# Kernel tuning notes

Hardware: AMD Instinct MI355X
Metric: run time of the kernel (lower is better)

The kernel has to match this reference:

```python
import jax, jax.numpy as jnp
import numpy as np

N = 20000      # nodes
E = 320000     # edges
GD = 256       # g_dim
H = 8          # head_n
D = 32         # head_d
XD = 256       # x_dim
PS = 4         # x_ps
HID = 512      # FF hidden (hardcoded in module)
EPS = 1e-5
SCALE = GD ** -0.5  # note: module scales by g_dim**-0.5, not head_d**-0.5


def layernorm(x, w, b):
    mu = jnp.mean(x, axis=-1, keepdims=True)
    var = jnp.var(x, axis=-1, keepdims=True)
    return (x - mu) * jax.lax.rsqrt(var + EPS) * w + b


def setup_inputs() -> dict:
    key = jax.random.key(0)
    ks = jax.random.split(key, 16)
    inp = {
        "x": jax.random.normal(ks[0], (N, XD, PS, PS), jnp.float32),
        "h": jax.random.normal(ks[1], (N, GD), jnp.float32),
        "src": jax.random.randint(ks[2], (E,), 0, N, jnp.int32),
        "dst": jax.random.randint(ks[3], (E,), 0, N, jnp.int32),
        # xproj conv (kernel covers full patch -> equivalent to a linear)
        "conv_w": jax.random.normal(ks[4], (GD, XD, PS, PS), jnp.float32) * 0.02,
        "conv_b": jnp.zeros((GD,), jnp.float32),
        # GraphT outer LayerNorm
        "norm_w": jnp.ones((GD,), jnp.float32),
        "norm_b": jnp.zeros((GD,), jnp.float32),
        # attention norm_in + projections
        "nin_w": jnp.ones((GD,), jnp.float32),
        "nin_b": jnp.zeros((GD,), jnp.float32),
        "w_qkv": jax.random.normal(ks[5], (3 * H * D, GD), jnp.float32) * 0.02,
        "w_out": jax.random.normal(ks[6], (GD, H * D), jnp.float32) * 0.02,
        "b_out": jnp.zeros((GD,), jnp.float32),
        # FeedForward: LayerNorm + Linear(GD,HID) + GELU + Linear(HID,GD)
        "ffn_w": jnp.ones((GD,), jnp.float32),
        "ffn_b": jnp.zeros((GD,), jnp.float32),
        "w1": jax.random.normal(ks[7], (HID, GD), jnp.float32) * 0.02,
        "b1": jnp.zeros((HID,), jnp.float32),
        "w2": jax.random.normal(ks[8], (GD, HID), jnp.float32) * 0.02,
        "b2": jnp.zeros((GD,), jnp.float32),
    }
    return inp


def reference(x, h, src, dst, conv_w, conv_b, norm_w, norm_b, nin_w, nin_b,
              w_qkv, w_out, b_out, ffn_w, ffn_b, w1, b1, w2, b2):
    # xproj: Conv2d with kernel == full spatial extent -> linear over flattened patch
    xp = x.reshape(N, XD * PS * PS) @ conv_w.reshape(GD, XD * PS * PS).T + conv_b  # [N, GD]

    hn = layernorm(h, norm_w, norm_b)  # GraphT.norm

    # --- GraphAttention ---
    s = layernorm(hn, nin_w, nin_b)                    # norm_in
    qkv = s @ w_qkv.T                                  # [N, 3*H*D]
    q, k, v = jnp.split(qkv, 3, axis=-1)
    q = q.reshape(N, H, D)
    k = k.reshape(N, H, D)
    v = v.reshape(N, H, D)

    # per-edge elementwise attention (DGL u_mul_v), scaled
    att = q[src] * k[dst] * SCALE                      # [E, H, D]
    # edge softmax over incoming edges of each destination, per (h, d) slot
    amax = jax.ops.segment_max(att, dst, num_segments=N)   # [N, H, D]
    e = jnp.exp(att - amax[dst])
    z = jax.ops.segment_sum(e, dst, num_segments=N)
    a = e / z[dst]                                     # [E, H, D]
    # weighted aggregation: sum over edges of v_src * att
    rst = jax.ops.segment_sum(v[src] * a, dst, num_segments=N)  # [N, H, D]

    attn_out = rst.reshape(N, H * D) @ w_out.T + b_out  # to_out (dropout=eval noop)

    # --- FeedForward (norm -> linear -> gelu -> linear) ---
    f = layernorm(attn_out, ffn_w, ffn_b)
    f = jax.nn.gelu(f @ w1.T + b1, approximate=False)
    f = f @ w2.T + b2

    out = f + hn + xp
    return out
```

## Files before the change

### kernel.cpp

```cpp
#include <hip/hip_runtime.h>
#include <hip/hip_bf16.h>
#include <math.h>

typedef __hip_bfloat16 bf16;
typedef __attribute__((ext_vector_type(8))) short bf16x8;
typedef __attribute__((ext_vector_type(4))) float f32x4;

#define N_NODES 20000
#define N_EDGES 320000
#define GD 256
#define HID 512
#define QKV3 768
#define XK 4096
#define SCALE 0.0625f
#define EPS 1e-5f

__device__ __forceinline__ float b2f(bf16 x) { return __bfloat162float(x); }
__device__ __forceinline__ bf16 f2b(float x) { return __float2bfloat16(x); }
__device__ __forceinline__ short f2bs(float x) {
    bf16 b = __float2bfloat16(x);
    union { bf16 b; short s; } u; u.b = b; return u.s;
}
__device__ __forceinline__ float ldf(const void* p, size_t i, int isbf) {
    return isbf ? __bfloat162float(((const bf16*)p)[i]) : ((const float*)p)[i];
}

typedef __attribute__((address_space(3))) void lds_void;
typedef __attribute__((address_space(1))) void glb_void;
__device__ __forceinline__ void gload_lds16(const void* g, void* l) {
    __builtin_amdgcn_global_load_lds((const glb_void*)g, (lds_void*)l, 16, 0, 0);
}

__global__ void detect_kernel(const void* __restrict__ normw, int* __restrict__ flag) {
    if (threadIdx.x == 0) {
        unsigned short u = ((const unsigned short*)normw)[0];
        *flag = (u == 0x3F80) ? 1 : 0;
    }
}

struct ConvArgs {
    const void* src[5];
    bf16* dst[5];
    int n[5];
};
__global__ void conv_bf16_all(ConvArgs a, const int* __restrict__ flag, bf16* __restrict__ cwt) {
    int i = blockIdx.x * 256 + threadIdx.x;
    int fl = *flag;
    #pragma unroll
    for (int s = 0; s < 5; ++s) {
        if (i < a.n[s]) {
            float v = ldf(a.src[s], i, fl);
            a.dst[s][i] = f2b(v);
            if (s == 0) {
                int r = i >> 12;
                int k = i & 4095;
                int T = k >> 5, slot = (k >> 3) & 3, e = k & 7;
                cwt[((size_t)T << 13) + (slot << 11) + (r << 3) + e] = f2b(v);
            }
            return;
        }
        i -= a.n[s];
    }
}

__global__ void count_kernel(const int* __restrict__ dst, int* __restrict__ deg) {
    int e = blockIdx.x * 256 + threadIdx.x;
    if (e < N_EDGES) atomicAdd(&deg[dst[e]], 1);
}

__global__ void scan_kernel(const int* __restrict__ deg, int* __restrict__ offsets,
                            int* __restrict__ cursor) {
    const int T = 1024;
    int t = threadIdx.x;
    int chunk = (N_NODES + T - 1) / T;
    int beg = t * chunk;
    int end = beg + chunk; if (end > N_NODES) end = N_NODES;
    int s = 0;
    for (int i = beg; i < end; ++i) s += deg[i];
    __shared__ int ls[T];
    ls[t] = s;
    __syncthreads();
    for (int off = 1; off < T; off <<= 1) {
        int v = (t >= off) ? ls[t - off] : 0;
        __syncthreads();
        ls[t] += v;
        __syncthreads();
    }
    int run = (t == 0) ? 0 : ls[t - 1];
    for (int i = beg; i < end; ++i) {
        offsets[i] = run; cursor[i] = run; run += deg[i];
    }
    if (t == T - 1) offsets[N_NODES] = run;
}

__global__ void fill_kernel(const int* __restrict__ src, const int* __restrict__ dst,
                            int* __restrict__ cursor, int* __restrict__ ssrc) {
    int e = blockIdx.x * 256 + threadIdx.x;
    if (e < N_EDGES) {
        int p = atomicAdd(&cursor[dst[e]], 1);
        ssrc[p] = src[e];
    }
}

__global__ void ln_fused_kernel(const void* __restrict__ h,
                                const void* __restrict__ nw, const void* __restrict__ nb,
                                const void* __restrict__ iw, const void* __restrict__ ib,
                                float* __restrict__ hn, bf16* __restrict__ s,
                                const int* __restrict__ flag) {
    int wave = threadIdx.x >> 6, lane = threadIdx.x & 63;
    int n = blockIdx.x * 4 + wave;
    int fl = *flag;
    size_t base = (size_t)n * GD;
    float x[4]; float sum = 0.f, sq = 0.f;
    #pragma unroll
    for (int i = 0; i < 4; ++i) {
        x[i] = ldf(h, base + lane + 64 * i, fl);
        sum += x[i]; sq += x[i] * x[i];
    }
    #pragma unroll
    for (int off = 32; off; off >>= 1) { sum += __shfl_xor(sum, off); sq += __shfl_xor(sq, off); }
    float mu = sum * (1.0f / GD);
    float rs = rsqrtf(sq * (1.0f / GD) - mu * mu + EPS);
    float y[4]; float s2 = 0.f, q2 = 0.f;
    #pragma unroll
    for (int i = 0; i < 4; ++i) {
        int j = lane + 64 * i;
        y[i] = (x[i] - mu) * rs * ldf(nw, j, fl) + ldf(nb, j, fl);
        hn[base + j] = y[i];
        s2 += y[i]; q2 += y[i] * y[i];
    }
    #pragma unroll
    for (int off = 32; off; off >>= 1) { s2 += __shfl_xor(s2, off); q2 += __shfl_xor(q2, off); }
    float mu2 = s2 * (1.0f / GD);
    float rs2 = rsqrtf(q2 * (1.0f / GD) - mu2 * mu2 + EPS);
    #pragma unroll
    for (int i = 0; i < 4; ++i) {
        int j = lane + 64 * i;
        s[base + j] = f2b((y[i] - mu2) * rs2 * ldf(iw, j, fl) + ldf(ib, j, fl));
    }
}

__global__ void ln_kernel(const bf16* __restrict__ in,
                          const void* __restrict__ w, const void* __restrict__ b,
                          bf16* __restrict__ out, const int* __restrict__ flag) {
    int wave = threadIdx.x >> 6, lane = threadIdx.x & 63;
    int n = blockIdx.x * 4 + wave;
    int fl = *flag;
    size_t base = (size_t)n * GD;
    float x[4]; float sum = 0.f, sq = 0.f;
    #pragma unroll
    for (int i = 0; i < 4; ++i) {
        x[i] = b2f(in[base + lane + 64 * i]);
        sum += x[i]; sq += x[i] * x[i];
    }
    #pragma unroll
    for (int off = 32; off; off >>= 1) { sum += __shfl_xor(sum, off); sq += __shfl_xor(sq, off); }
    float mu = sum * (1.0f / GD);
    float rs = rsqrtf(sq * (1.0f / GD) - mu * mu + EPS);
    #pragma unroll
    for (int i = 0; i < 4; ++i) {
        int j = lane + 64 * i;
        out[base + j] = f2b((x[i] - mu) * rs * ldf(w, j, fl) + ldf(b, j, fl));
    }
}

__global__ void attn_kernel(const bf16* __restrict__ qkv, const int* __restrict__ offsets,
                            const int* __restrict__ ssrc, bf16* __restrict__ rst) {
    int n = blockIdx.x;
    int j = threadIdx.x;
    float kj = b2f(qkv[(size_t)n * QKV3 + GD + j]) * SCALE;
    int beg = offsets[n], end = offsets[n + 1];
    float m = -INFINITY, l = 0.f, acc = 0.f;
    for (int e = beg; e < end; ++e) {
        int sI = ssrc[e];
        const bf16* qrow = qkv + (size_t)sI * QKV3;
        float a = b2f(qrow[j]) * kj;
        float vv = b2f(qrow[2 * GD + j]);
        float mn = fmaxf(m, a);
        float c = __expf(m - mn);
        float p = __expf(a - mn);
        l = l * c + p;
        acc = acc * c + p * vv;
        m = mn;
    }
    rst[(size_t)n * GD + j] = f2b(end > beg ? acc / l : 0.f);
}

__launch_bounds__(512, 4)
__global__ void xproj_pipe(const float* __restrict__ A, const bf16* __restrict__ Bt,
                           const float* __restrict__ bias, float* __restrict__ C,
                           const int* __restrict__ flag) {
    if (*flag) return;
    constexpr int BK = 32;
    __shared__ __align__(16) float As[2][4096];
    __shared__ __align__(16) bf16  Bs[2][8192];
    const int m0 = blockIdx.x * 128;
    const int lane = threadIdx.x & 63;
    const int wave = threadIdx.x >> 6;
    const int quad = lane >> 4;
    const int l16 = lane & 15;
    const int wm = (wave & 1) * 64;
    const int wn = (wave >> 1) * 64;
    const int kc = XK / gridDim.z;
    const int kbeg = blockIdx.z * kc;
    const int nt = kc / BK;

    f32x4 acc[4][4] = {};

    auto stage = [&](int buf, int t) {
        int k0 = kbeg + t * BK;
        #pragma unroll
        for (int s = 0; s < 2; ++s) {
            int ki = wave * 2 + s;
            int row = ki * 8 + (lane >> 3);
            int gr = m0 + row; if (gr >= N_NODES) gr = N_NODES - 1;
            int gslot = (lane & 7) ^ (row & 7);
            gload_lds16(A + (size_t)gr * XK + k0 + gslot * 4,
                        (char*)(&As[buf][0]) + ki * 1024);
        }
        size_t tb = (size_t)(k0 >> 5) * 16384;
        #pragma unroll
        for (int s = 0; s < 2; ++s) {
            int ki = wave * 2 + s;
            gload_lds16((const char*)Bt + tb + ki * 1024 + lane * 16,
                        (char*)(&Bs[buf][0]) + ki * 1024);
        }
    };

    auto compute = [&](int buf) {
        bf16x8 bfm[4];
        #pragma unroll
        for (int j = 0; j < 4; ++j)
            bfm[j] = *(const bf16x8*)(&Bs[buf][quad * 2048 + (wn + j * 16 + l16) * 8]);
        const f32x4* ap = (const f32x4*)(&As[buf][0]);
        #pragma unroll
        for (int i = 0; i < 4; ++i) {
            int r = wm + i * 16 + l16;
            f32x4 a0 = ap[r * 8 + ((quad * 2) ^ (r & 7))];
            f32x4 a1 = ap[r * 8 + ((quad * 2 + 1) ^ (r & 7))];
            bf16x8 v;
            v[0] = f2bs(a0[0]); v[1] = f2bs(a0[1]); v[2] = f2bs(a0[2]); v[3] = f2bs(a0[3]);
            v[4] = f2bs(a1[0]); v[5] = f2bs(a1[1]); v[6] = f2bs(a1[2]); v[7] = f2bs(a1[3]);
            #pragma unroll
            for (int j = 0; j < 4; ++j)
                acc[i][j] = __builtin_amdgcn_mfma_f32_16x16x32_bf16(v, bfm[j], acc[i][j], 0, 0, 0);
        }
    };

    stage(0, 0);
    stage(1, 1);
    for (int t = 0; t < nt - 1; ++t) {
        asm volatile("s_waitcnt vmcnt(4)" ::: "memory");
        asm volatile("s_barrier" ::: "memory");
        compute(t & 1);
        asm volatile("s_waitcnt lgkmcnt(0)" ::: "memory");
        __builtin_amdgcn_sched_barrier(0);
        asm volatile("s_barrier" ::: "memory");
        if (t + 2 < nt) stage(t & 1, t + 2);
    }
    asm volatile("s_waitcnt vmcnt(0)" ::: "memory");
    asm volatile("s_barrier" ::: "memory");
    compute((nt - 1) & 1);

    #pragma unroll
    for (int i = 0; i < 4; ++i) {
        #pragma unroll
        for (int j = 0; j < 4; ++j) {
            int col = wn + j * 16 + l16;
            float bv = (blockIdx.z == 0) ? bias[col] : 0.0f;
            #pragma unroll
            for (int r = 0; r < 4; ++r) {
                int gr = m0 + wm + i * 16 + quad * 4 + r;
                if (gr >= N_NODES) continue;
                atomicAdd(&C[(size_t)gr * GD + col], acc[i][j][r] + bv);
            }
        }
    }
}

template<int EPI, int DYNA>
__launch_bounds__(256)
__global__ void gemm_bt(const void* __restrict__ A, const bf16* __restrict__ B,
                        const void* __restrict__ bias, void* __restrict__ Cout,
                        const float* __restrict__ add0, const float* __restrict__ add1,
                        int M, int Nn, int K, const int* __restrict__ flag) {
    const int fl = *flag;
    if (DYNA == 2 && fl == 0) return;
    constexpr int BM = 128, BN = 128, BK = 64, LDW = BK + 8;
    __shared__ bf16 As[BM * LDW];
    __shared__ bf16 Bs[BN * LDW];
    const int m0 = blockIdx.x * BM;
    const int n0 = blockIdx.y * BN;
    const int tid = threadIdx.x;
    const int lane = tid & 63;
    const int wave = tid >> 6;
    const int quad = lane >> 4;
    const int l16 = lane & 15;
    const int wm = (wave & 1) * 64;
    const int wn = (wave >> 1) * 64;

    const int kc = K / gridDim.z;
    const int kbeg = blockIdx.z * kc;
    const int kend = kbeg + kc;

    f32x4 acc[4][4] = {};

    for (int k0 = kbeg; k0 < kend; k0 += BK) {
        #pragma unroll
        for (int p = 0; p < 4; ++p) {
            int l = p * 256 + tid;
            int row = l >> 3;
            int ko = (l & 7) * 8;
            int gr = m0 + row; gr = gr < M ? gr : M - 1;
            if (!DYNA || fl) {
                *(int4*)(&As[row * LDW + ko]) =
                    *(const int4*)((const bf16*)A + (size_t)gr * K + k0 + ko);
            } else {
                const float* Af = (const float*)A + (size_t)gr * K + k0 + ko;
                float4 lo = *(const float4*)(Af);
                float4 hi = *(const float4*)(Af + 4);
                bf16x8 v;
                v[0] = f2bs(lo.x); v[1] = f2bs(lo.y); v[2] = f2bs(lo.z); v[3] = f2bs(lo.w);
                v[4] = f2bs(hi.x); v[5] = f2bs(hi.y); v[6] = f2bs(hi.z); v[7] = f2bs(hi.w);
                *(bf16x8*)(&As[row * LDW + ko]) = v;
            }
            *(int4*)(&Bs[row * LDW + ko]) = *(const int4*)(B + (size_t)(n0 + row) * K + k0 + ko);
        }
        __syncthreads();
        #pragma unroll
        for (int kk = 0; kk < BK; kk += 32) {
            bf16x8 af[4], bfm[4];
            #pragma unroll
            for (int i = 0; i < 4; ++i)
                af[i] = *(const bf16x8*)(&As[(wm + i * 16 + l16) * LDW + kk + quad * 8]);
            #pragma unroll
            for (int j = 0; j < 4; ++j)
                bfm[j] = *(const bf16x8*)(&Bs[(wn + j * 16 + l16) * LDW + kk + quad * 8]);
            #pragma unroll
            for (int i = 0; i < 4; ++i)
                #pragma unroll
                for (int j = 0; j < 4; ++j)
                    acc[i][j] = __builtin_amdgcn_mfma_f32_16x16x32_bf16(af[i], bfm[j], acc[i][j], 0, 0, 0);
        }
        __syncthreads();
    }

    #pragma unroll
    for (int i = 0; i < 4; ++i) {
        #pragma unroll
        for (int j = 0; j < 4; ++j) {
            int col = n0 + wn + j * 16 + l16;
            float bv = bias ? ldf(bias, col, fl) : 0.0f;
            if (EPI == 4 && blockIdx.z != 0) bv = 0.0f;
            #pragma unroll
            for (int r = 0; r < 4; ++r) {
                int gr = m0 + wm + i * 16 + quad * 4 + r;
                if (gr >= M) continue;
                float v = acc[i][j][r] + bv;
                size_t idx = (size_t)gr * Nn + col;
                if (EPI == 2) v = 0.5f * v * (1.0f + erff(v * 0.70710678118f));
                if (EPI == 3) v += add0[idx] + add1[idx];
                if (EPI == 0)      ((float*)Cout)[idx] = v;
                else if (EPI == 3) { if (fl) ((bf16*)Cout)[idx] = f2b(v); else ((float*)Cout)[idx] = v; }
                else if (EPI == 4) atomicAdd(&((float*)Cout)[idx], v);
                else               ((bf16*)Cout)[idx] = f2b(v);
            }
        }
    }
}

extern "C" void kernel_launch(void* const* d_in, const int* in_sizes, int n_in,
                              void* d_out, int out_size, void* d_ws, size_t ws_size,
                              hipStream_t stream) {
    const void* x      = d_in[0];
    const void* h      = d_in[1];
    const int*  src    = (const int*)d_in[2];
    const int*  dst    = (const int*)d_in[3];
    const void* conv_w = d_in[4];
    const void* conv_b = d_in[5];
    const void* norm_w = d_in[6];
    const void* norm_b = d_in[7];
    const void* nin_w  = d_in[8];
    const void* nin_b  = d_in[9];
    const void* w_qkv  = d_in[10];
    const void* w_out  = d_in[11];
    const void* b_out  = d_in[12];
    const void* ffn_w  = d_in[13];
    const void* ffn_b  = d_in[14];
    const void* w1     = d_in[15];
    const void* b1     = d_in[16];
    const void* w2     = d_in[17];
    const void* b2     = d_in[18];

    char* w = (char*)d_ws;
    float* xp   = (float*)w; w += (size_t)N_NODES * GD * 4;
    float* hn   = (float*)w; w += (size_t)N_NODES * GD * 4;
    bf16*  s    = (bf16*)w;  w += (size_t)N_NODES * GD * 2;
    bf16*  qkv  = (bf16*)w;  w += (size_t)N_NODES * QKV3 * 2;
    bf16*  rst  = (bf16*)w;  w += (size_t)N_NODES * GD * 2;
    bf16*  attn = (bf16*)w;  w += (size_t)N_NODES * GD * 2;
    bf16*  cw    = (bf16*)w; w += (size_t)4096 * 256 * 2;
    bf16*  cwt   = (bf16*)w; w += (size_t)4096 * 256 * 2;
    bf16*  wqkvb = (bf16*)w; w += (size_t)768 * 256 * 2;
    bf16*  woutb = (bf16*)w; w += (size_t)256 * 256 * 2;
    bf16*  w1b   = (bf16*)w; w += (size_t)512 * 256 * 2;
    bf16*  w2b   = (bf16*)w; w += (size_t)256 * 512 * 2;
    int* deg     = (int*)w;  w += (size_t)N_NODES * 4;
    int* cursor  = (int*)w;  w += (size_t)N_NODES * 4;
    int* offsets = (int*)w;  w += (size_t)(N_NODES + 4) * 4;
    int* ssrc    = (int*)w;  w += (size_t)N_EDGES * 4;
    int* flag    = (int*)w;  w += 16;
    bf16* fln = s;
    bf16* f1  = qkv;

    detect_kernel<<<1, 64, 0, stream>>>(norm_w, flag);
    ConvArgs ca;
    ca.src[0] = conv_w; ca.dst[0] = cw;    ca.n[0] = 4096 * 256;
    ca.src[1] = w_qkv;  ca.dst[1] = wqkvb; ca.n[1] = 768 * 256;
    ca.src[2] = w_out;  ca.dst[2] = woutb; ca.n[2] = 256 * 256;
    ca.src[3] = w1;     ca.dst[3] = w1b;   ca.n[3] = 512 * 256;
    ca.src[4] = w2;     ca.dst[4] = w2b;   ca.n[4] = 256 * 512;
    int conv_total = ca.n[0] + ca.n[1] + ca.n[2] + ca.n[3] + ca.n[4];
    conv_bf16_all<<<(conv_total + 255) / 256, 256, 0, stream>>>(ca, flag, cwt);

    hipMemsetAsync(deg, 0, N_NODES * sizeof(int), stream);
    count_kernel<<<(N_EDGES + 255) / 256, 256, 0, stream>>>(dst, deg);
    scan_kernel<<<1, 1024, 0, stream>>>(deg, offsets, cursor);
    fill_kernel<<<(N_EDGES + 255) / 256, 256, 0, stream>>>(src, dst, cursor, ssrc);

    ln_fused_kernel<<<N_NODES / 4, 256, 0, stream>>>(h, norm_w, norm_b, nin_w, nin_b, hn, s, flag);

    dim3 blk(256);
    hipMemsetAsync(xp, 0, (size_t)N_NODES * GD * 4, stream);
    xproj_pipe<<<dim3(157, 1, 4), dim3(512), 0, stream>>>((const float*)x, cwt, (const float*)conv_b, xp, flag);
    gemm_bt<4, 2><<<dim3(157, 2, 4), blk, 0, stream>>>(x, cw, conv_b, xp, nullptr, nullptr, N_NODES, GD, 4096, flag);
    gemm_bt<1, 0><<<dim3(157, 6), blk, 0, stream>>>(s, wqkvb, nullptr, qkv, nullptr, nullptr, N_NODES, QKV3, GD, flag);
    attn_kernel<<<N_NODES, 256, 0, stream>>>(qkv, offsets, ssrc, rst);
    gemm_bt<1, 0><<<dim3(157, 2), blk, 0, stream>>>(rst, woutb, b_out, attn, nullptr, nullptr, N_NODES, GD, GD, flag);
    ln_kernel<<<N_NODES / 4, 256, 0, stream>>>(attn, ffn_w, ffn_b, fln, flag);
    gemm_bt<2, 0><<<dim3(157, 4), blk, 0, stream>>>(fln, w1b, b1, f1, nullptr, nullptr, N_NODES, HID, GD, flag);
    gemm_bt<3, 0><<<dim3(157, 2), blk, 0, stream>>>(f1, w2b, b2, d_out, xp, hn, N_NODES, GD, HID, flag);
}
```

Measured before the change: 929.7 us.

## Load xproj weight fragments directly into registers and shrink M tile to 64

```diff
diff --git a/kernel.cpp b/kernel.cpp
--- a/kernel.cpp
+++ b/kernel.cpp
@@ -186,81 +186,95 @@
     rst[(size_t)n * GD + j] = f2b(end > beg ? acc / l : 0.f);
 }
 
-__launch_bounds__(512, 4)
-__global__ void xproj_pipe(const float* __restrict__ A, const bf16* __restrict__ Bt,
-                           const float* __restrict__ bias, float* __restrict__ C,
-                           const int* __restrict__ flag) {
+#define LOADB(R0, R1, R2, R3, T) {                                                        \
+    const bf16* pb_ = Bt + (((size_t)((kbeg >> 5) + (T))) << 13) + (q << 11)              \
+                         + (((size_t)wn + l16) << 3);                                     \
+    R0 = *(const int4*)(pb_);                                                             \
+    R1 = *(const int4*)(pb_ + 128);                                                       \
+    R2 = *(const int4*)(pb_ + 256);                                                       \
+    R3 = *(const int4*)(pb_ + 384); }
+
+#define STAGEA(BUF, T) {                                                                  \
+    int k0_ = kbeg + (T) * 32;                                                            \
+    {   int ki = wave * 2;                                                                \
+        int row = ki * 8 + (lane >> 3);                                                   \
+        int gr = m0 + row; if (gr >= N_NODES) gr = N_NODES - 1;                           \
+        int gs = (lane & 7) ^ (row & 7);                                                  \
+        gload_lds16(A + (size_t)gr * XK + k0_ + gs * 4, (char*)As + (BUF) * 8192 + ki * 1024); } \
+    {   int ki = wave * 2 + 1;                                                            \
+        int row = ki * 8 + (lane >> 3);                                                   \
+        int gr = m0 + row; if (gr >= N_NODES) gr = N_NODES - 1;                           \
+        int gs = (lane & 7) ^ (row & 7);                                                  \
+        gload_lds16(A + (size_t)gr * XK + k0_ + gs * 4, (char*)As + (BUF) * 8192 + ki * 1024); } }
+
+__device__ __forceinline__ void xp_mfma_row(const f32x4* ap, int r, int quad,
+                                            bf16x8 b0, bf16x8 b1, bf16x8 b2, bf16x8 b3,
+                                            f32x4* accRow) {
+    f32x4 a0 = ap[r * 8 + ((quad * 2) ^ (r & 7))];
+    f32x4 a1 = ap[r * 8 + ((quad * 2 + 1) ^ (r & 7))];
+    bf16x8 v;
+    v[0] = f2bs(a0[0]); v[1] = f2bs(a0[1]); v[2] = f2bs(a0[2]); v[3] = f2bs(a0[3]);
+    v[4] = f2bs(a1[0]); v[5] = f2bs(a1[1]); v[6] = f2bs(a1[2]); v[7] = f2bs(a1[3]);
+    accRow[0] = __builtin_amdgcn_mfma_f32_16x16x32_bf16(v, b0, accRow[0], 0, 0, 0);
+    accRow[1] = __builtin_amdgcn_mfma_f32_16x16x32_bf16(v, b1, accRow[1], 0, 0, 0);
+    accRow[2] = __builtin_amdgcn_mfma_f32_16x16x32_bf16(v, b2, accRow[2], 0, 0, 0);
+    accRow[3] = __builtin_amdgcn_mfma_f32_16x16x32_bf16(v, b3, accRow[3], 0, 0, 0);
+}
+
+#define COMPUTE(BUF, R0, R1, R2, R3) {                                                    \
+    const f32x4* ap_ = (const f32x4*)((const char*)As + (BUF) * 8192);                    \
+    bf16x8 b0_ = __builtin_bit_cast(bf16x8, R0);                                          \
+    bf16x8 b1_ = __builtin_bit_cast(bf16x8, R1);                                          \
+    bf16x8 b2_ = __builtin_bit_cast(bf16x8, R2);                                          \
+    bf16x8 b3_ = __builtin_bit_cast(bf16x8, R3);                                          \
+    xp_mfma_row(ap_,      l16, quad, b0_, b1_, b2_, b3_, &acc[0][0]);                     \
+    xp_mfma_row(ap_, 16 + l16, quad, b0_, b1_, b2_, b3_, &acc[1][0]);                     \
+    xp_mfma_row(ap_, 32 + l16, quad, b0_, b1_, b2_, b3_, &acc[2][0]);                     \
+    xp_mfma_row(ap_, 48 + l16, quad, b0_, b1_, b2_, b3_, &acc[3][0]); }
+
+__launch_bounds__(256, 3)
+__global__ void xproj_v4(const float* __restrict__ A, const bf16* __restrict__ Bt,
+                         const float* __restrict__ bias, float* __restrict__ C,
+                         const int* __restrict__ flag) {
     if (*flag) return;
-    constexpr int BK = 32;
-    __shared__ __align__(16) float As[2][4096];
-    __shared__ __align__(16) bf16  Bs[2][8192];
-    const int m0 = blockIdx.x * 128;
+    __shared__ __align__(16) float As[2][2048];
+    const int m0 = blockIdx.x * 64;
     const int lane = threadIdx.x & 63;
     const int wave = threadIdx.x >> 6;
     const int quad = lane >> 4;
     const int l16 = lane & 15;
-    const int wm = (wave & 1) * 64;
-    const int wn = (wave >> 1) * 64;
+    const int q = quad;
+    const int wn = wave * 64;
     const int kc = XK / gridDim.z;
     const int kbeg = blockIdx.z * kc;
-    const int nt = kc / BK;
+    const int nt = kc / 32;
 
     f32x4 acc[4][4] = {};
-
-    auto stage = [&](int buf, int t) {
-        int k0 = kbeg + t * BK;
-        #pragma unroll
-        for (int s = 0; s < 2; ++s) {
-            int ki = wave * 2 + s;
-            int row = ki * 8 + (lane >> 3);
-            int gr = m0 + row; if (gr >= N_NODES) gr = N_NODES - 1;
-            int gslot = (lane & 7) ^ (row & 7);
-            gload_lds16(A + (size_t)gr * XK + k0 + gslot * 4,
-                        (char*)(&As[buf][0]) + ki * 1024);
-        }
-        size_t tb = (size_t)(k0 >> 5) * 16384;
-        #pragma unroll
-        for (int s = 0; s < 2; ++s) {
-            int ki = wave * 2 + s;
-            gload_lds16((const char*)Bt + tb + ki * 1024 + lane * 16,
-                        (char*)(&Bs[buf][0]) + ki * 1024);
-        }
-    };
-
-    auto compute = [&](int buf) {
-        bf16x8 bfm[4];
-        #pragma unroll
-        for (int j = 0; j < 4; ++j)
-            bfm[j] = *(const bf16x8*)(&Bs[buf][quad * 2048 + (wn + j * 16 + l16) * 8]);
-        const f32x4* ap = (const f32x4*)(&As[buf][0]);
-        #pragma unroll
-        for (int i = 0; i < 4; ++i) {
-            int r = wm + i * 16 + l16;
-            f32x4 a0 = ap[r * 8 + ((quad * 2) ^ (r & 7))];
-            f32x4 a1 = ap[r * 8 + ((quad * 2 + 1) ^ (r & 7))];
-            bf16x8 v;
-            v[0] = f2bs(a0[0]); v[1] = f2bs(a0[1]); v[2] = f2bs(a0[2]); v[3] = f2bs(a0[3]);
-            v[4] = f2bs(a1[0]); v[5] = f2bs(a1[1]); v[6] = f2bs(a1[2]); v[7] = f2bs(a1[3]);
-            #pragma unroll
-            for (int j = 0; j < 4; ++j)
-                acc[i][j] = __builtin_amdgcn_mfma_f32_16x16x32_bf16(v, bfm[j], acc[i][j], 0, 0, 0);
-        }
-    };
-
-    stage(0, 0);
-    stage(1, 1);
-    for (int t = 0; t < nt - 1; ++t) {
-        asm volatile("s_waitcnt vmcnt(4)" ::: "memory");
+    int4 bA0, bA1, bA2, bA3, bB0, bB1, bB2, bB3;
+
+    STAGEA(0, 0);
+    LOADB(bA0, bA1, bA2, bA3, 0);
+    STAGEA(1, 1);
+
+    for (int t = 0; t < nt; t += 2) {
+        asm volatile("s_waitcnt vmcnt(2)" ::: "memory");
         asm volatile("s_barrier" ::: "memory");
-        compute(t & 1);
-        asm volatile("s_waitcnt lgkmcnt(0)" ::: "memory");
+        { int Tn = t + 1 < nt ? t + 1 : nt - 1; LOADB(bB0, bB1, bB2, bB3, Tn); }
+        __builtin_amdgcn_sched_barrier(0);
+        COMPUTE(0, bA0, bA1, bA2, bA3);
         __builtin_amdgcn_sched_barrier(0);
         asm volatile("s_barrier" ::: "memory");
-        if (t + 2 < nt) stage(t & 1, t + 2);
+        { int Tn = t + 2 < nt ? t + 2 : nt - 1; STAGEA(0, Tn); }
+        asm volatile("s_waitcnt vmcnt(2)" ::: "memory");
+        asm volatile("s_barrier" ::: "memory");
+        { int Tn = t + 2 < nt ? t + 2 : nt - 1; LOADB(bA0, bA1, bA2, bA3, Tn); }
+        __builtin_amdgcn_sched_barrier(0);
+        COMPUTE(1, bB0, bB1, bB2, bB3);
+        __builtin_amdgcn_sched_barrier(0);
+        asm volatile("s_barrier" ::: "memory");
+        { int Tn = t + 3 < nt ? t + 3 : nt - 1; STAGEA(1, Tn); }
     }
     asm volatile("s_waitcnt vmcnt(0)" ::: "memory");
-    asm volatile("s_barrier" ::: "memory");
-    compute((nt - 1) & 1);
 
     #pragma unroll
     for (int i = 0; i < 4; ++i) {
@@ -270,7 +284,7 @@
             float bv = (blockIdx.z == 0) ? bias[col] : 0.0f;
             #pragma unroll
             for (int r = 0; r < 4; ++r) {
-                int gr = m0 + wm + i * 16 + quad * 4 + r;
+                int gr = m0 + i * 16 + quad * 4 + r;
                 if (gr >= N_NODES) continue;
                 atomicAdd(&C[(size_t)gr * GD + col], acc[i][j][r] + bv);
             }
@@ -432,7 +446,7 @@
 
     dim3 blk(256);
     hipMemsetAsync(xp, 0, (size_t)N_NODES * GD * 4, stream);
-    xproj_pipe<<<dim3(157, 1, 4), dim3(512), 0, stream>>>((const float*)x, cwt, (const float*)conv_b, xp, flag);
+    xproj_v4<<<dim3(313, 1, 4), blk, 0, stream>>>((const float*)x, cwt, (const float*)conv_b, xp, flag);
     gemm_bt<4, 2><<<dim3(157, 2, 4), blk, 0, stream>>>(x, cw, conv_b, xp, nullptr, nullptr, N_NODES, GD, 4096, flag);
     gemm_bt<1, 0><<<dim3(157, 6), blk, 0, stream>>>(s, wqkvb, nullptr, qkv, nullptr, nullptr, N_NODES, QKV3, GD, flag);
     attn_kernel<<<N_NODES, 256, 0, stream>>>(qkv, offsets, ssrc, rst);
```

Result: no change. 921.8 us (-0.9%).

## Replace atomic split-K xproj with two-way split into separate buffers summed in epilogue

Applied to the files above, without the earlier changes.

```diff
diff --git a/kernel.cpp b/kernel.cpp
--- a/kernel.cpp
+++ b/kernel.cpp
@@ -186,93 +186,78 @@
     rst[(size_t)n * GD + j] = f2b(end > beg ? acc / l : 0.f);
 }
 
-__launch_bounds__(512, 4)
-__global__ void xproj_pipe(const float* __restrict__ A, const bf16* __restrict__ Bt,
-                           const float* __restrict__ bias, float* __restrict__ C,
-                           const int* __restrict__ flag) {
+__launch_bounds__(256, 3)
+__global__ void xproj_v5(const float* __restrict__ A, const bf16* __restrict__ Bt,
+                         const float* __restrict__ bias, float* __restrict__ C0,
+                         float* __restrict__ C1, const int* __restrict__ flag) {
     if (*flag) return;
-    constexpr int BK = 32;
-    __shared__ __align__(16) float As[2][4096];
-    __shared__ __align__(16) bf16  Bs[2][8192];
-    const int m0 = blockIdx.x * 128;
+    __shared__ __align__(16) float As[4096];
+    __shared__ __align__(16) bf16  Bs[16384];
+    const int m0 = blockIdx.x * 64;
     const int lane = threadIdx.x & 63;
     const int wave = threadIdx.x >> 6;
-    const int quad = lane >> 4;
+    const int q = lane >> 4;
     const int l16 = lane & 15;
-    const int wm = (wave & 1) * 64;
-    const int wn = (wave >> 1) * 64;
-    const int kc = XK / gridDim.z;
+    const int wn = wave * 64;
+    const int kc = XK >> 1;
     const int kbeg = blockIdx.z * kc;
-    const int nt = kc / BK;
+    const int nt = kc / 64;
 
     f32x4 acc[4][4] = {};
 
-    auto stage = [&](int buf, int t) {
-        int k0 = kbeg + t * BK;
-        #pragma unroll
-        for (int s = 0; s < 2; ++s) {
-            int ki = wave * 2 + s;
-            int row = ki * 8 + (lane >> 3);
+    for (int t = 0; t < nt; ++t) {
+        int k0 = kbeg + t * 64;
+        #pragma unroll
+        for (int s = 0; s < 4; ++s) {
+            int ki = wave * 4 + s;
+            int row = ki * 4 + (lane >> 4);
             int gr = m0 + row; if (gr >= N_NODES) gr = N_NODES - 1;
-            int gslot = (lane & 7) ^ (row & 7);
-            gload_lds16(A + (size_t)gr * XK + k0 + gslot * 4,
-                        (char*)(&As[buf][0]) + ki * 1024);
-        }
-        size_t tb = (size_t)(k0 >> 5) * 16384;
-        #pragma unroll
-        for (int s = 0; s < 2; ++s) {
-            int ki = wave * 2 + s;
-            gload_lds16((const char*)Bt + tb + ki * 1024 + lane * 16,
-                        (char*)(&Bs[buf][0]) + ki * 1024);
-        }
-    };
-
-    auto compute = [&](int buf) {
-        bf16x8 bfm[4];
-        #pragma unroll
-        for (int j = 0; j < 4; ++j)
-            bfm[j] = *(const bf16x8*)(&Bs[buf][quad * 2048 + (wn + j * 16 + l16) * 8]);
-        const f32x4* ap = (const f32x4*)(&As[buf][0]);
-        #pragma unroll
-        for (int i = 0; i < 4; ++i) {
-            int r = wm + i * 16 + l16;
-            f32x4 a0 = ap[r * 8 + ((quad * 2) ^ (r & 7))];
-            f32x4 a1 = ap[r * 8 + ((quad * 2 + 1) ^ (r & 7))];
-            bf16x8 v;
-            v[0] = f2bs(a0[0]); v[1] = f2bs(a0[1]); v[2] = f2bs(a0[2]); v[3] = f2bs(a0[3]);
-            v[4] = f2bs(a1[0]); v[5] = f2bs(a1[1]); v[6] = f2bs(a1[2]); v[7] = f2bs(a1[3]);
+            int ls = lane & 15;
+            int gs = (ls & 8) | ((ls & 7) ^ (row & 7));
+            gload_lds16(A + (size_t)gr * XK + k0 + gs * 4, (char*)As + ki * 1024);
+        }
+        const char* bsrc = (const char*)(Bt + (((size_t)(k0 >> 5)) << 13));
+        #pragma unroll
+        for (int s = 0; s < 8; ++s) {
+            int ki = wave * 8 + s;
+            gload_lds16(bsrc + ki * 1024 + lane * 16, (char*)Bs + ki * 1024);
+        }
+        __syncthreads();
+        #pragma unroll
+        for (int h = 0; h < 2; ++h) {
+            bf16x8 bfm[4];
             #pragma unroll
             for (int j = 0; j < 4; ++j)
-                acc[i][j] = __builtin_amdgcn_mfma_f32_16x16x32_bf16(v, bfm[j], acc[i][j], 0, 0, 0);
-        }
-    };
-
-    stage(0, 0);
-    stage(1, 1);
-    for (int t = 0; t < nt - 1; ++t) {
-        asm volatile("s_waitcnt vmcnt(4)" ::: "memory");
-        asm volatile("s_barrier" ::: "memory");
-        compute(t & 1);
-        asm volatile("s_waitcnt lgkmcnt(0)" ::: "memory");
-        __builtin_amdgcn_sched_barrier(0);
-        asm volatile("s_barrier" ::: "memory");
-        if (t + 2 < nt) stage(t & 1, t + 2);
-    }
-    asm volatile("s_waitcnt vmcnt(0)" ::: "memory");
-    asm volatile("s_barrier" ::: "memory");
-    compute((nt - 1) & 1);
-
+                bfm[j] = *(const bf16x8*)(&Bs[h * 8192 + q * 2048 + (wn + j * 16 + l16) * 8]);
+            const f32x4* ap = (const f32x4*)As;
+            #pragma unroll
+            for (int i = 0; i < 4; ++i) {
+                int r = i * 16 + l16;
+                f32x4 a0 = ap[r * 16 + h * 8 + ((2 * q) ^ (r & 7))];
+                f32x4 a1 = ap[r * 16 + h * 8 + ((2 * q + 1) ^ (r & 7))];
+                bf16x8 v;
+                v[0] = f2bs(a0[0]); v[1] = f2bs(a0[1]); v[2] = f2bs(a0[2]); v[3] = f2bs(a0[3]);
+                v[4] = f2bs(a1[0]); v[5] = f2bs(a1[1]); v[6] = f2bs(a1[2]); v[7] = f2bs(a1[3]);
+                #pragma unroll
+                for (int j = 0; j < 4; ++j)
+                    acc[i][j] = __builtin_amdgcn_mfma_f32_16x16x32_bf16(v, bfm[j], acc[i][j], 0, 0, 0);
+            }
+        }
+        __syncthreads();
+    }
+
+    float* C = (blockIdx.z == 0) ? C0 : C1;
     #pragma unroll
     for (int i = 0; i < 4; ++i) {
         #pragma unroll
         for (int j = 0; j < 4; ++j) {
             int col = wn + j * 16 + l16;
-            float bv = (blockIdx.z == 0) ? bias[col] : 0.0f;
+            float bv = (blockIdx.z == 0 && bias) ? bias[col] : 0.0f;
             #pragma unroll
             for (int r = 0; r < 4; ++r) {
-                int gr = m0 + wm + i * 16 + quad * 4 + r;
+                int gr = m0 + i * 16 + q * 4 + r;
                 if (gr >= N_NODES) continue;
-                atomicAdd(&C[(size_t)gr * GD + col], acc[i][j][r] + bv);
+                C[(size_t)gr * GD + col] = acc[i][j][r] + bv;
             }
         }
     }
@@ -283,6 +268,7 @@
 __global__ void gemm_bt(const void* __restrict__ A, const bf16* __restrict__ B,
                         const void* __restrict__ bias, void* __restrict__ Cout,
                         const float* __restrict__ add0, const float* __restrict__ add1,
+                        const float* __restrict__ add2,
                         int M, int Nn, int K, const int* __restrict__ flag) {
     const int fl = *flag;
     if (DYNA == 2 && fl == 0) return;
@@ -299,13 +285,9 @@
     const int wm = (wave & 1) * 64;
     const int wn = (wave >> 1) * 64;
 
-    const int kc = K / gridDim.z;
-    const int kbeg = blockIdx.z * kc;
-    const int kend = kbeg + kc;
-
     f32x4 acc[4][4] = {};
 
-    for (int k0 = kbeg; k0 < kend; k0 += BK) {
+    for (int k0 = 0; k0 < K; k0 += BK) {
         #pragma unroll
         for (int p = 0; p < 4; ++p) {
             int l = p * 256 + tid;
@@ -351,7 +333,6 @@
         for (int j = 0; j < 4; ++j) {
             int col = n0 + wn + j * 16 + l16;
             float bv = bias ? ldf(bias, col, fl) : 0.0f;
-            if (EPI == 4 && blockIdx.z != 0) bv = 0.0f;
             #pragma unroll
             for (int r = 0; r < 4; ++r) {
                 int gr = m0 + wm + i * 16 + quad * 4 + r;
@@ -359,10 +340,9 @@
                 float v = acc[i][j][r] + bv;
                 size_t idx = (size_t)gr * Nn + col;
                 if (EPI == 2) v = 0.5f * v * (1.0f + erff(v * 0.70710678118f));
-                if (EPI == 3) v += add0[idx] + add1[idx];
+                if (EPI == 3) v += add0[idx] + add1[idx] + add2[idx];
                 if (EPI == 0)      ((float*)Cout)[idx] = v;
                 else if (EPI == 3) { if (fl) ((bf16*)Cout)[idx] = f2b(v); else ((float*)Cout)[idx] = v; }
-                else if (EPI == 4) atomicAdd(&((float*)Cout)[idx], v);
                 else               ((bf16*)Cout)[idx] = f2b(v);
             }
         }
@@ -393,7 +373,8 @@
     const void* b2     = d_in[18];
 
     char* w = (char*)d_ws;
-    float* xp   = (float*)w; w += (size_t)N_NODES * GD * 4;
+    float* xp0  = (float*)w; w += (size_t)N_NODES * GD * 4;
+    float* xp1  = (float*)w; w += (size_t)N_NODES * GD * 4;
     float* hn   = (float*)w; w += (size_t)N_NODES * GD * 4;
     bf16*  s    = (bf16*)w;  w += (size_t)N_NODES * GD * 2;
     bf16*  qkv  = (bf16*)w;  w += (size_t)N_NODES * QKV3 * 2;
@@ -431,13 +412,13 @@
     ln_fused_kernel<<<N_NODES / 4, 256, 0, stream>>>(h, norm_w, norm_b, nin_w, nin_b, hn, s, flag);
 
     dim3 blk(256);
-    hipMemsetAsync(xp, 0, (size_t)N_NODES * GD * 4, stream);
-    xproj_pipe<<<dim3(157, 1, 4), dim3(512), 0, stream>>>((const float*)x, cwt, (const float*)conv_b, xp, flag);
-    gemm_bt<4, 2><<<dim3(157, 2, 4), blk, 0, stream>>>(x, cw, conv_b, xp, nullptr, nullptr, N_NODES, GD, 4096, flag);
-    gemm_bt<1, 0><<<dim3(157, 6), blk, 0, stream>>>(s, wqkvb, nullptr, qkv, nullptr, nullptr, N_NODES, QKV3, GD, flag);
+    hipMemsetAsync(xp1, 0, (size_t)N_NODES * GD * 4, stream);
+    xproj_v5<<<dim3(313, 1, 2), blk, 0, stream>>>((const float*)x, cwt, (const float*)conv_b, xp0, xp1, flag);
+    gemm_bt<0, 2><<<dim3(157, 2), blk, 0, stream>>>(x, cw, conv_b, xp0, nullptr, nullptr, nullptr, N_NODES, GD, 4096, flag);
+    gemm_bt<1, 0><<<dim3(157, 6), blk, 0, stream>>>(s, wqkvb, nullptr, qkv, nullptr, nullptr, nullptr, N_NODES, QKV3, GD, flag);
     attn_kernel<<<N_NODES, 256, 0, stream>>>(qkv, offsets, ssrc, rst);
-    gemm_bt<1, 0><<<dim3(157, 2), blk, 0, stream>>>(rst, woutb, b_out, attn, nullptr, nullptr, N_NODES, GD, GD, flag);
+    gemm_bt<1, 0><<<dim3(157, 2), blk, 0, stream>>>(rst, woutb, b_out, attn, nullptr, nullptr, nullptr, N_NODES, GD, GD, flag);
     ln_kernel<<<N_NODES / 4, 256, 0, stream>>>(attn, ffn_w, ffn_b, fln, flag);
-    gemm_bt<2, 0><<<dim3(157, 4), blk, 0, stream>>>(fln, w1b, b1, f1, nullptr, nullptr, N_NODES, HID, GD, flag);
-    gemm_bt<3, 0><<<dim3(157, 2), blk, 0, stream>>>(f1, w2b, b2, d_out, xp, hn, N_NODES, GD, HID, flag);
-}
+    gemm_bt<2, 0><<<dim3(157, 4), blk, 0, stream>>>(fln, w1b, b1, f1, nullptr, nullptr, nullptr, N_NODES, HID, GD, flag);
+    gemm_bt<3, 0><<<dim3(157, 2), blk, 0, stream>>>(f1, w2b, b2, d_out, xp0, xp1, hn, N_NODES, GD, HID, flag);
+}
```

After: 866.9 us. -6.8%, faster.
